# Kernel tuning notes

Hardware: AMD Instinct MI355X
Metric: run time of the kernel (lower is better)

The kernel has to match this reference:

```python
import jax, jax.numpy as jnp
import numpy as np

M = 50000
N = 50000
H = 32
C = 128
K = 15          # sum(shell_sizes) = 1 + 14
GROUPS = 8
CPG = C // GROUPS  # 16
RADIUS = 1.2
SIGMA = 0.9
INF = 1.0e6


def _make_kernel_points():
    # fixed='center': first point at origin, rest uniformly in the ball of radius RADIUS
    rng = np.random.RandomState(42)
    pts = rng.randn(K, 3).astype(np.float32)
    pts /= np.linalg.norm(pts, axis=1, keepdims=True) + 1e-9
    r = rng.rand(K, 1).astype(np.float32) ** (1.0 / 3.0)
    pts = pts * r * RADIUS
    pts[0] = 0.0
    return jnp.asarray(pts)


def setup_inputs() -> dict:
    key = jax.random.key(0)
    ks = jax.random.split(key, 8)
    q_pts = jax.random.normal(ks[0], (M, 3), jnp.float32) * 5.0
    s_pts = q_pts + 0.0  # M == N case (same point set)
    s_feats = jax.random.normal(ks[1], (N, C), jnp.float32)
    neighb_inds = jax.random.randint(ks[2], (M, H), 0, N)
    da_scale = jax.random.uniform(ks[3], (M,), jnp.float32, 0.5, 1.5)
    # learned params
    weights = jax.random.normal(ks[4], (K, C), jnp.float32) * (1.0 / np.sqrt(C))
    w1 = jax.random.normal(ks[5], (C, C), jnp.float32) * (1.0 / np.sqrt(C))
    b1 = jnp.zeros((C,), jnp.float32)
    w2 = jax.random.normal(ks[6], (C, K * CPG), jnp.float32) * (1.0 / np.sqrt(C))
    kernel_points = _make_kernel_points()
    return {
        "q_pts": q_pts, "s_pts": s_pts, "s_feats": s_feats,
        "neighb_inds": neighb_inds, "da_scale": da_scale,
        "weights": weights, "w1": w1, "b1": b1, "w2": w2,
        "kernel_points": kernel_points,
    }


def reference(q_pts, s_pts, s_feats, neighb_inds, da_scale,
              weights, w1, b1, w2, kernel_points):
    # --- neighbor feature gather (padded shadow row of zeros) ---
    padded = jnp.concatenate([s_feats, jnp.zeros((1, C), s_feats.dtype)], axis=0)
    neighbor_feats = padded[neighb_inds]               # [M, H, C]

    # --- modulations from pooled feats (M == N -> pooled = s_feats) ---
    pooled = s_feats
    h = jax.nn.leaky_relu(pooled @ w1 + b1, 0.1)
    modulations = jax.nn.sigmoid(h @ w2)               # [M, K*CPG]
    modulations = modulations.reshape(-1, K, CPG, 1)
    conv_w = weights.reshape(1, K, CPG, GROUPS) * modulations
    conv_w = conv_w.reshape(-1, K, C)                  # [M, K, C]

    # --- density-adaptive kernel-point influences (no-grad in original) ---
    s_pad = jnp.concatenate([s_pts, jnp.full((1, 3), INF, s_pts.dtype)], axis=0)
    neighbors = s_pad[neighb_inds] - q_pts[:, None, :]            # [M, H, 3]
    scaled_kp = kernel_points[None] * da_scale[:, None, None]     # [M, K, 3]
    diff = neighbors[:, :, None, :] - scaled_kp[:, None, :, :]    # [M, H, K, 3]
    sq_d = jnp.sum(diff * diff, axis=-1)                          # [M, H, K]
    nn_sq = jnp.min(sq_d, axis=2)                                 # [M, H]
    nn_idx = jnp.argmin(sq_d, axis=2)                             # [M, H]
    infl = jnp.clip(1.0 - jnp.sqrt(nn_sq) / SIGMA, 0.0)           # linear mode
    infl = jax.lax.stop_gradient(infl)

    # --- gather per-neighbor kernel weights, modulate, aggregate ---
    nw = jnp.take_along_axis(conv_w, nn_idx[:, :, None], axis=1)  # [M, H, C]
    nw = nw * infl[:, :, None]
    return jnp.sum(neighbor_feats * nw, axis=1)                   # [M, C]
```

## Files before the change

### kernel.cpp

```cpp
#include <hip/hip_runtime.h>
#include <cstddef>
#include <cstdint>

namespace {
constexpr int H_N    = 32;
constexpr int C_F    = 128;
constexpr int K_P    = 15;
constexpr int MODC   = 240;
constexpr int ROWS_B = 64;
constexpr int LDS_SZ  = ROWS_B * MODC * 2;
}

typedef __attribute__((ext_vector_type(8))) short short8v;
typedef __attribute__((ext_vector_type(4))) float f32x4;

__device__ __forceinline__ unsigned short bf16_hi(float f) {
    unsigned u = __builtin_bit_cast(unsigned, f);
    unsigned r = (u + 0x7FFFu + ((u >> 16) & 1u)) >> 16;
    return (unsigned short)r;
}
__device__ __forceinline__ float bf16_f(unsigned short h) {
    unsigned u = ((unsigned)h) << 16;
    return __builtin_bit_cast(float, u);
}

__global__ __launch_bounds__(256)
void split_w_kernel(const float* __restrict__ w1, const float* __restrict__ w2,
                    unsigned short* __restrict__ w1t, unsigned short* __restrict__ w2t)
{
    const int i = blockIdx.x * 256 + threadIdx.x;
    if (i < C_F * C_F) {
        const int c = i >> 7, j = i & 127;
        w1t[j * C_F + c] = bf16_hi(w1[i]);
    }
    const int i2 = i - C_F * C_F;
    if (i2 >= 0 && i2 < C_F * MODC) {
        const int c = i2 / MODC, j = i2 - c * MODC;
        w2t[j * C_F + c] = bf16_hi(w2[i2]);
    }
}

__global__ __launch_bounds__(512, 4)
void fused_kernel(const float* __restrict__ q_pts,
                  const float* __restrict__ s_pts,
                  const float* __restrict__ s_feats,
                  const int* __restrict__ nbi,
                  const float* __restrict__ da_scale,
                  const float* __restrict__ weights,
                  const float* __restrict__ kp,
                  const unsigned short* __restrict__ w1t,
                  const unsigned short* __restrict__ w2t,
                  const float* __restrict__ b1,
                  float* __restrict__ out,
                  int M)
{
    __shared__ __align__(16) unsigned char lds[LDS_SZ];

    const int t  = threadIdx.x;
    const int r0 = blockIdx.x * ROWS_B;
    const int rows = min(M - r0, ROWS_B);

    {
        const int row = t >> 3;
        const int k0  = (t & 7) << 4;
        const float4* src = reinterpret_cast<const float4*>(
            s_feats + (size_t)(r0 + row) * C_F + k0);
        #pragma unroll
        for (int s = 0; s < 2; ++s) {
            float v[8];
            if (row < rows) {
                const float4 a = src[s * 2 + 0];
                const float4 b = src[s * 2 + 1];
                v[0] = a.x; v[1] = a.y; v[2] = a.z; v[3] = a.w;
                v[4] = b.x; v[5] = b.y; v[6] = b.z; v[7] = b.w;
            } else {
                #pragma unroll
                for (int e = 0; e < 8; ++e) v[e] = 0.f;
            }
            short8v hv;
            #pragma unroll
            for (int e = 0; e < 8; ++e) hv[e] = (short)bf16_hi(v[e]);
            const unsigned addr = (unsigned)((row * 256 + (k0 + s * 8) * 2) ^ ((row & 7) << 4));
            *reinterpret_cast<short8v*>(lds + addr) = hv;
        }
    }
    __syncthreads();

    const int wave = t >> 6, lane = t & 63;
    const int wc = wave;
    const int g  = lane >> 4;
    const int ln = lane & 15;

    {
        const int col = wc * 16 + ln;
        f32x4 acc[4];
        {
            const float b = b1[col];
            #pragma unroll
            for (int rt = 0; rt < 4; ++rt) acc[rt] = f32x4{b, b, b, b};
        }
        #pragma unroll
        for (int ks = 0; ks < 4; ++ks) {
            short8v a[4];
            #pragma unroll
            for (int rt = 0; rt < 4; ++rt) {
                const int row = rt * 16 + ln;
                const unsigned addr = (unsigned)((row * 256 + (ks * 32 + g * 8) * 2) ^ ((row & 7) << 4));
                a[rt] = *reinterpret_cast<const short8v*>(lds + addr);
            }
            const short8v b = *reinterpret_cast<const short8v*>(
                w1t + (size_t)col * C_F + ks * 32 + g * 8);
            #pragma unroll
            for (int rt = 0; rt < 4; ++rt)
                acc[rt] = __builtin_amdgcn_mfma_f32_16x16x32_bf16(a[rt], b, acc[rt], 0, 0, 0);
        }
        __syncthreads();

        #pragma unroll
        for (int rt = 0; rt < 4; ++rt) {
            #pragma unroll
            for (int r = 0; r < 4; ++r) {
                float v = acc[rt][r];
                v = v > 0.f ? v : 0.1f * v;
                const int row = rt * 16 + g * 4 + r;
                const unsigned addr = (unsigned)((row * 256 + col * 2) ^ ((row & 7) << 4));
                *reinterpret_cast<unsigned short*>(lds + addr) = bf16_hi(v);
            }
        }
    }
    __syncthreads();

    f32x4 acc2[4][2];
    #pragma unroll
    for (int rt = 0; rt < 4; ++rt)
        #pragma unroll
        for (int cs = 0; cs < 2; ++cs) acc2[rt][cs] = f32x4{0.f, 0.f, 0.f, 0.f};

    #pragma unroll
    for (int ks = 0; ks < 4; ++ks) {
        short8v a[4];
        #pragma unroll
        for (int rt = 0; rt < 4; ++rt) {
            const int row = rt * 16 + ln;
            const unsigned addr = (unsigned)((row * 256 + (ks * 32 + g * 8) * 2) ^ ((row & 7) << 4));
            a[rt] = *reinterpret_cast<const short8v*>(lds + addr);
        }
        #pragma unroll
        for (int cs = 0; cs < 2; ++cs) {
            const int ctile = wc + 8 * cs;
            if (ctile < K_P) {
                const int col = ctile * 16 + ln;
                const short8v b = *reinterpret_cast<const short8v*>(
                    w2t + (size_t)col * C_F + ks * 32 + g * 8);
                #pragma unroll
                for (int rt = 0; rt < 4; ++rt)
                    acc2[rt][cs] = __builtin_amdgcn_mfma_f32_16x16x32_bf16(a[rt], b, acc2[rt][cs], 0, 0, 0);
            }
        }
    }
    #pragma unroll
    for (int rt = 0; rt < 4; ++rt)
        #pragma unroll
        for (int cs = 0; cs < 2; ++cs)
            #pragma unroll
            for (int r = 0; r < 4; ++r)
                acc2[rt][cs][r] = 1.f / (1.f + __expf(-acc2[rt][cs][r]));

    __syncthreads();

    #pragma unroll
    for (int rt = 0; rt < 4; ++rt) {
        #pragma unroll
        for (int cs = 0; cs < 2; ++cs) {
            const int ctile = wc + 8 * cs;
            if (ctile < K_P) {
                const int col = ctile * 16 + ln;
                #pragma unroll
                for (int r = 0; r < 4; ++r) {
                    const int row = rt * 16 + g * 4 + r;
                    *reinterpret_cast<unsigned short*>(
                        lds + row * (MODC * 2) + col * 2) = bf16_hi(acc2[rt][cs][r]);
                }
            }
        }
    }
    __syncthreads();

    const int hl   = lane & 31;
    const int half = lane >> 5;
    const int c0   = hl << 2;
    for (int i = 0; i < 4; ++i) {
        const int ql = i * 16 + wave * 2 + half;
        const bool valid = ql < rows;
        const int mq = r0 + ql;

        int   idx = 0, nn = 0;
        float fl  = 0.f;
        if (valid) {
            const float qx = q_pts[mq * 3 + 0];
            const float qy = q_pts[mq * 3 + 1];
            const float qz = q_pts[mq * 3 + 2];
            const float das = da_scale[mq];
            idx = nbi[(size_t)mq * H_N + hl];
            const float sx = s_pts[idx * 3 + 0];
            const float sy = s_pts[idx * 3 + 1];
            const float sz = s_pts[idx * 3 + 2];
            const float dx = __fsub_rn(sx, qx);
            const float dy = __fsub_rn(sy, qy);
            const float dz = __fsub_rn(sz, qz);
            const float dd = __fadd_rn(__fadd_rn(__fmul_rn(dx, dx), __fmul_rn(dy, dy)),
                                       __fmul_rn(dz, dz));
            const float reach = 0.9f + 1.2f * das;
            if (dd < reach * reach) {
                float best = 3.4e38f; int bi = 0;
                #pragma unroll
                for (int k = 0; k < K_P; ++k) {
                    const float ex = __fsub_rn(dx, __fmul_rn(kp[k * 3 + 0], das));
                    const float ey = __fsub_rn(dy, __fmul_rn(kp[k * 3 + 1], das));
                    const float ez = __fsub_rn(dz, __fmul_rn(kp[k * 3 + 2], das));
                    const float d2 = __fadd_rn(__fadd_rn(__fmul_rn(ex, ex), __fmul_rn(ey, ey)),
                                               __fmul_rn(ez, ez));
                    if (d2 < best) { best = d2; bi = k; }
                }
                const float f = 1.f - sqrtf(best) / 0.9f;
                fl = fmaxf(f, 0.f);
                nn = bi;
            }
        }

        const unsigned long long mask = __ballot(fl > 0.f);
        unsigned long long mymask = half ? (mask & 0xFFFFFFFF00000000ull)
                                         : (mask & 0x00000000FFFFFFFFull);
        float4 acc = {0.f, 0.f, 0.f, 0.f};
        while (mymask) {
            const int hb = __builtin_ctzll(mymask);
            mymask &= mymask - 1;
            const int   ih = __shfl(idx, hb);
            const int   nh = __shfl(nn, hb);
            const float fh = __shfl(fl, hb);
            const float4 fv = *reinterpret_cast<const float4*>(s_feats + (size_t)ih * C_F + c0);
            const float4 wv = *reinterpret_cast<const float4*>(weights + nh * C_F + c0);
            const float  mv = bf16_f(*reinterpret_cast<const unsigned short*>(
                lds + ql * (MODC * 2) + (nh * 16 + (hl >> 1)) * 2));
            const float  s  = fh * mv;
            acc.x = fmaf(fv.x * wv.x, s, acc.x);
            acc.y = fmaf(fv.y * wv.y, s, acc.y);
            acc.z = fmaf(fv.z * wv.z, s, acc.z);
            acc.w = fmaf(fv.w * wv.w, s, acc.w);
        }
        if (valid)
            *reinterpret_cast<float4*>(out + (size_t)mq * C_F + c0) = acc;
    }
}

extern "C" void kernel_launch(void* const* d_in, const int* in_sizes, int n_in,
                              void* d_out, int out_size, void* d_ws, size_t ws_size,
                              hipStream_t stream)
{
    const float* q_pts  = (const float*)d_in[0];
    const float* s_pts  = (const float*)d_in[1];
    const float* s_feat = (const float*)d_in[2];
    const int*   nbi    = (const int*)d_in[3];
    const float* da     = (const float*)d_in[4];
    const float* wts    = (const float*)d_in[5];
    const float* w1     = (const float*)d_in[6];
    const float* b1     = (const float*)d_in[7];
    const float* w2     = (const float*)d_in[8];
    const float* kp     = (const float*)d_in[9];
    float* out = (float*)d_out;

    const int M = in_sizes[4];

    unsigned short* w1t = (unsigned short*)d_ws;
    unsigned short* w2t = w1t + C_F * C_F;

    const int nsplit = (C_F * C_F + C_F * MODC + 255) / 256;
    split_w_kernel<<<dim3(nsplit), 256, 0, stream>>>(w1, w2, w1t, w2t);

    const int nb = (M + ROWS_B - 1) / ROWS_B;
    fused_kernel<<<dim3(nb), 512, 0, stream>>>(
        q_pts, s_pts, s_feat, nbi, da, wts, kp, w1t, w2t, b1, out, M);
}
```

Baseline: 42.83 us.

## Compact active query rows before running the modulation MLP and aggregation

Splits the fused kernel in two. A geometry pass computes each query's nearest kernel point and influence, writes zeros directly for rows with no positive influence, and compacts the remaining rows through an atomic counter into an index list with packed neighbor and influence data. The second kernel then runs the bf16 MFMA modulation MLP and the aggregation only for these compacted rows, avoiding matmul work for queries whose output is zero. The price is an extra launch, a workspace round trip for the packed data, an indirect gather of feature rows, and a grid that is still sized for every row, so blocks past the active count exit immediately.

```diff
diff --git a/kernel.cpp b/kernel.cpp
--- a/kernel.cpp
+++ b/kernel.cpp
@@ -8,7 +8,7 @@
 constexpr int K_P    = 15;
 constexpr int MODC   = 240;
 constexpr int ROWS_B = 64;
-constexpr int LDS_SZ  = ROWS_B * MODC * 2;
+constexpr int LDS_SZ = ROWS_B * MODC * 2;
 }
 
 typedef __attribute__((ext_vector_type(8))) short short8v;
@@ -26,9 +26,11 @@
 
 __global__ __launch_bounds__(256)
 void split_w_kernel(const float* __restrict__ w1, const float* __restrict__ w2,
-                    unsigned short* __restrict__ w1t, unsigned short* __restrict__ w2t)
+                    unsigned short* __restrict__ w1t, unsigned short* __restrict__ w2t,
+                    int* __restrict__ counter)
 {
     const int i = blockIdx.x * 256 + threadIdx.x;
+    if (i == 0) *counter = 0;
     if (i < C_F * C_F) {
         const int c = i >> 7, j = i & 127;
         w1t[j * C_F + c] = bf16_hi(w1[i]);
@@ -40,31 +42,100 @@
     }
 }
 
+__global__ __launch_bounds__(256)
+void geom_kernel(const float* __restrict__ q_pts,
+                 const float* __restrict__ s_pts,
+                 const int* __restrict__ nbi,
+                 const float* __restrict__ da_scale,
+                 const float* __restrict__ kp,
+                 int* __restrict__ counter,
+                 int* __restrict__ qidx,
+                 unsigned* __restrict__ pk,
+                 float* __restrict__ gfl,
+                 float* __restrict__ out,
+                 int M)
+{
+    const int t    = threadIdx.x;
+    const int lane = t & 63;
+    const int r    = blockIdx.x * 4 + (t >> 6);
+    if (r >= M) return;
+
+    int   idx = 0, nn = 0;
+    float fl  = 0.f;
+    if (lane < H_N) {
+        const float qx = q_pts[r * 3 + 0];
+        const float qy = q_pts[r * 3 + 1];
+        const float qz = q_pts[r * 3 + 2];
+        const float das = da_scale[r];
+        idx = nbi[(size_t)r * H_N + lane];
+        const float sx = s_pts[idx * 3 + 0];
+        const float sy = s_pts[idx * 3 + 1];
+        const float sz = s_pts[idx * 3 + 2];
+        const float dx = __fsub_rn(sx, qx);
+        const float dy = __fsub_rn(sy, qy);
+        const float dz = __fsub_rn(sz, qz);
+        const float dd = __fadd_rn(__fadd_rn(__fmul_rn(dx, dx), __fmul_rn(dy, dy)),
+                                   __fmul_rn(dz, dz));
+        const float reach = 0.9f + 1.2f * das;
+        if (dd < reach * reach) {
+            float best = 3.4e38f; int bi = 0;
+            #pragma unroll
+            for (int k = 0; k < K_P; ++k) {
+                const float ex = __fsub_rn(dx, __fmul_rn(kp[k * 3 + 0], das));
+                const float ey = __fsub_rn(dy, __fmul_rn(kp[k * 3 + 1], das));
+                const float ez = __fsub_rn(dz, __fmul_rn(kp[k * 3 + 2], das));
+                const float d2 = __fadd_rn(__fadd_rn(__fmul_rn(ex, ex), __fmul_rn(ey, ey)),
+                                           __fmul_rn(ez, ez));
+                if (d2 < best) { best = d2; bi = k; }
+            }
+            const float f = 1.f - sqrtf(best) / 0.9f;
+            fl = fmaxf(f, 0.f);
+            nn = bi;
+        }
+    }
+
+    const unsigned long long mask = __ballot(fl > 0.f);
+    if (mask == 0ull) {
+        reinterpret_cast<float2*>(out + (size_t)r * C_F)[lane] = make_float2(0.f, 0.f);
+        return;
+    }
+    int pos = 0;
+    if (lane == 0) pos = atomicAdd(counter, 1);
+    pos = __shfl(pos, 0);
+    if (lane == 0) qidx[pos] = r;
+    if (lane < H_N) {
+        pk [(size_t)pos * H_N + lane] = (unsigned)idx | ((unsigned)nn << 20);
+        gfl[(size_t)pos * H_N + lane] = fl;
+    }
+}
+
 __global__ __launch_bounds__(512, 4)
-void fused_kernel(const float* __restrict__ q_pts,
-                  const float* __restrict__ s_pts,
-                  const float* __restrict__ s_feats,
-                  const int* __restrict__ nbi,
-                  const float* __restrict__ da_scale,
-                  const float* __restrict__ weights,
-                  const float* __restrict__ kp,
-                  const unsigned short* __restrict__ w1t,
-                  const unsigned short* __restrict__ w2t,
-                  const float* __restrict__ b1,
-                  float* __restrict__ out,
-                  int M)
+void active_kernel(const float* __restrict__ s_feats,
+                   const float* __restrict__ weights,
+                   const unsigned short* __restrict__ w1t,
+                   const unsigned short* __restrict__ w2t,
+                   const float* __restrict__ b1,
+                   const int* __restrict__ counter,
+                   const int* __restrict__ qidx,
+                   const unsigned* __restrict__ pk,
+                   const float* __restrict__ gfl,
+                   float* __restrict__ out)
 {
     __shared__ __align__(16) unsigned char lds[LDS_SZ];
 
-    const int t  = threadIdx.x;
+    const int count = *counter;
     const int r0 = blockIdx.x * ROWS_B;
-    const int rows = min(M - r0, ROWS_B);
+    const int rows = min(count - r0, ROWS_B);
+    if (rows <= 0) return;
+
+    const int t = threadIdx.x;
 
     {
         const int row = t >> 3;
         const int k0  = (t & 7) << 4;
+        const int src_m = (row < rows) ? qidx[r0 + row] : 0;
         const float4* src = reinterpret_cast<const float4*>(
-            s_feats + (size_t)(r0 + row) * C_F + k0);
+            s_feats + (size_t)src_m * C_F + k0);
         #pragma unroll
         for (int s = 0; s < 2; ++s) {
             float v[8];
@@ -192,40 +263,15 @@
     for (int i = 0; i < 4; ++i) {
         const int ql = i * 16 + wave * 2 + half;
         const bool valid = ql < rows;
-        const int mq = r0 + ql;
+        const int pos = r0 + ql;
 
         int   idx = 0, nn = 0;
         float fl  = 0.f;
         if (valid) {
-            const float qx = q_pts[mq * 3 + 0];
-            const float qy = q_pts[mq * 3 + 1];
-            const float qz = q_pts[mq * 3 + 2];
-            const float das = da_scale[mq];
-            idx = nbi[(size_t)mq * H_N + hl];
-            const float sx = s_pts[idx * 3 + 0];
-            const float sy = s_pts[idx * 3 + 1];
-            const float sz = s_pts[idx * 3 + 2];
-            const float dx = __fsub_rn(sx, qx);
-            const float dy = __fsub_rn(sy, qy);
-            const float dz = __fsub_rn(sz, qz);
-            const float dd = __fadd_rn(__fadd_rn(__fmul_rn(dx, dx), __fmul_rn(dy, dy)),
-                                       __fmul_rn(dz, dz));
-            const float reach = 0.9f + 1.2f * das;
-            if (dd < reach * reach) {
-                float best = 3.4e38f; int bi = 0;
-                #pragma unroll
-                for (int k = 0; k < K_P; ++k) {
-                    const float ex = __fsub_rn(dx, __fmul_rn(kp[k * 3 + 0], das));
-                    const float ey = __fsub_rn(dy, __fmul_rn(kp[k * 3 + 1], das));
-                    const float ez = __fsub_rn(dz, __fmul_rn(kp[k * 3 + 2], das));
-                    const float d2 = __fadd_rn(__fadd_rn(__fmul_rn(ex, ex), __fmul_rn(ey, ey)),
-                                               __fmul_rn(ez, ez));
-                    if (d2 < best) { best = d2; bi = k; }
-                }
-                const float f = 1.f - sqrtf(best) / 0.9f;
-                fl = fmaxf(f, 0.f);
-                nn = bi;
-            }
+            const unsigned p = pk[(size_t)pos * H_N + hl];
+            idx = (int)(p & 0xFFFFFu);
+            nn  = (int)(p >> 20);
+            fl  = gfl[(size_t)pos * H_N + hl];
         }
 
         const unsigned long long mask = __ballot(fl > 0.f);
@@ -248,8 +294,10 @@
             acc.z = fmaf(fv.z * wv.z, s, acc.z);
             acc.w = fmaf(fv.w * wv.w, s, acc.w);
         }
-        if (valid)
+        if (valid) {
+            const int mq = qidx[pos];
             *reinterpret_cast<float4*>(out + (size_t)mq * C_F + c0) = acc;
+        }
     }
 }
 
@@ -273,11 +321,20 @@
 
     unsigned short* w1t = (unsigned short*)d_ws;
     unsigned short* w2t = w1t + C_F * C_F;
+    size_t off = ((size_t)(C_F * C_F + C_F * MODC) * sizeof(unsigned short) + 255) & ~(size_t)255;
+    int* counter = (int*)((char*)d_ws + off);           off += 256;
+    int* qidx    = (int*)((char*)d_ws + off);           off += (size_t)M * 4;
+    off = (off + 255) & ~(size_t)255;
+    unsigned* pk = (unsigned*)((char*)d_ws + off);      off += (size_t)M * H_N * 4;
+    float* gfl   = (float*)((char*)d_ws + off);
 
     const int nsplit = (C_F * C_F + C_F * MODC + 255) / 256;
-    split_w_kernel<<<dim3(nsplit), 256, 0, stream>>>(w1, w2, w1t, w2t);
+    split_w_kernel<<<dim3(nsplit), 256, 0, stream>>>(w1, w2, w1t, w2t, counter);
+
+    geom_kernel<<<dim3((M + 3) / 4), 256, 0, stream>>>(
+        q_pts, s_pts, nbi, da, kp, counter, qidx, pk, gfl, out, M);
 
     const int nb = (M + ROWS_B - 1) / ROWS_B;
-    fused_kernel<<<dim3(nb), 512, 0, stream>>>(
-        q_pts, s_pts, s_feat, nbi, da, wts, kp, w1t, w2t, b1, out, M);
-}
+    active_kernel<<<dim3(nb), 512, 0, stream>>>(
+        s_feat, wts, w1t, w2t, b1, counter, qidx, pk, gfl, out);
+}
```

New measurement: 78.50 us. 1.83x slower.
